# Kernel optimization log

Hardware: AMD Instinct MI355X
Metric: run time of the kernel (lower is better)

## Reference

```python
import jax, jax.numpy as jnp
import numpy as np

T, B, I, H, L = 1024, 64, 512, 512, 2


def _gru_layer(x_seq, h0, w_ih, w_hh, b_ih, b_hh):
    # x_seq: [T, B, in], h0: [B, H]
    # Precompute input-side gates for all timesteps in one big GEMM.
    gx = jnp.einsum('tbi,gi->tbg', x_seq, w_ih) + b_ih  # [T, B, 3H]

    def step(h, gx_t):
        gh = h @ w_hh.T + b_hh                 # [B, 3H]
        i_r, i_z, i_n = jnp.split(gx_t, 3, axis=-1)
        h_r, h_z, h_n = jnp.split(gh, 3, axis=-1)
        r = jax.nn.sigmoid(i_r + h_r)
        z = jax.nn.sigmoid(i_z + h_z)
        n = jnp.tanh(i_n + r * h_n)
        hy = n + z * (h - n)                   # newgate + inputgate*(hx - newgate)
        return hy, hy

    hT, out = jax.lax.scan(step, h0, gx)
    return out, hT  # out: [T, B, H]


def setup_inputs() -> dict:
    key = jax.random.key(0)
    ks = jax.random.split(key, 10)
    stdv = 1.0 / np.sqrt(H)
    u = lambda k, shp: jax.random.uniform(k, shp, jnp.float32, -stdv, stdv)
    return {
        'x': jax.random.normal(ks[0], (T, B, I), jnp.float32),
        'hx': jax.random.normal(ks[1], (L, B, H), jnp.float32),
        'w_ih_0': u(ks[2], (3 * H, I)),
        'w_hh_0': u(ks[3], (3 * H, H)),
        'b_ih_0': u(ks[4], (3 * H,)),
        'b_hh_0': u(ks[5], (3 * H,)),
        'w_ih_1': u(ks[6], (3 * H, H)),
        'w_hh_1': u(ks[7], (3 * H, H)),
        'b_ih_1': u(ks[8], (3 * H,)),
        'b_hh_1': u(ks[9], (3 * H,)),
    }


def reference(x, hx, w_ih_0, w_hh_0, b_ih_0, b_hh_0, w_ih_1, w_hh_1, b_ih_1, b_hh_1):
    out0, h0T = _gru_layer(x, hx[0], w_ih_0, w_hh_0, b_ih_0, b_hh_0)
    out1, h1T = _gru_layer(out0, hx[1], w_ih_1, w_hh_1, b_ih_1, b_hh_1)
    output = out1                         # [T, B, H] (batch_first=False)
    output_hs = jnp.stack([h0T, h1T], 0)  # [L, B, H]
    return output, output_hs
```

## Files before the change

### kernel.cpp

```cpp
#include <hip/hip_runtime.h>
#include <cstdint>
#include <cstddef>

#define T_N 1024
#define B_N 64
#define I_N 512
#define H_N 512
#define G3  (3*H_N)
#define NBLK 256

typedef _Float16 f16;
typedef _Float16 f16x2 __attribute__((ext_vector_type(2)));
typedef unsigned long long ull;

#define SLOT(d) (((d)+2)&1)
#define TAG1(d) ((((d)+2)>>1)&1)

__device__ __forceinline__ f16x2 mkh2(float a, float b) {
  f16x2 v; v.x = (_Float16)a; v.y = (_Float16)b; return v;
}
__device__ __forceinline__ f16x2 bch2(unsigned int u) {
  return __builtin_bit_cast(f16x2, u);
}
__device__ __forceinline__ float fdot2_(f16x2 a, f16x2 b, float c) {
#if __has_builtin(__builtin_amdgcn_fdot2)
  return __builtin_amdgcn_fdot2(a, b, c, false);
#else
  return fmaf((float)a.x, (float)b.x, fmaf((float)a.y, (float)b.y, c));
#endif
}
__device__ __forceinline__ float sigm_(float x) { return 1.f / (1.f + __expf(-x)); }
__device__ __forceinline__ float tanhf_(float x) {
  float xx = fminf(15.f, fmaxf(-15.f, x));
  float e = __expf(2.f * xx);
  return (e - 1.f) / (e + 1.f);
}

__global__ __launch_bounds__(256) void gemm_nt(
    const float* __restrict__ A,
    const float* __restrict__ W,
    const float* __restrict__ bias,
    float* __restrict__ C,
    int M, int N, int K)
{
  __shared__ float As[32][68];
  __shared__ float Ws[32][68];
  const int tid = threadIdx.x;
  const int n0 = blockIdx.x * 64;
  const int m0 = blockIdx.y * 64;
  const int ty = tid >> 4;
  const int tx = tid & 15;

  float acc[4][4];
#pragma unroll
  for (int i = 0; i < 4; ++i)
#pragma unroll
    for (int jj = 0; jj < 4; ++jj) acc[i][jj] = 0.f;

  for (int k0 = 0; k0 < K; k0 += 32) {
#pragma unroll
    for (int i = 0; i < 2; ++i) {
      int idx = tid + i * 256;
      int r   = idx >> 3;
      int c4  = idx & 7;
      float4 va = *(const float4*)(A + (size_t)(m0 + r) * K + k0 + c4 * 4);
      As[c4*4+0][r] = va.x; As[c4*4+1][r] = va.y;
      As[c4*4+2][r] = va.z; As[c4*4+3][r] = va.w;
      float4 vw = *(const float4*)(W + (size_t)(n0 + r) * K + k0 + c4 * 4);
      Ws[c4*4+0][r] = vw.x; Ws[c4*4+1][r] = vw.y;
      Ws[c4*4+2][r] = vw.z; Ws[c4*4+3][r] = vw.w;
    }
    __syncthreads();
#pragma unroll
    for (int k = 0; k < 32; ++k) {
      float4 a = *(const float4*)&As[k][ty * 4];
      float4 w = *(const float4*)&Ws[k][tx * 4];
      acc[0][0] += a.x*w.x; acc[0][1] += a.x*w.y; acc[0][2] += a.x*w.z; acc[0][3] += a.x*w.w;
      acc[1][0] += a.y*w.x; acc[1][1] += a.y*w.y; acc[1][2] += a.y*w.z; acc[1][3] += a.y*w.w;
      acc[2][0] += a.z*w.x; acc[2][1] += a.z*w.y; acc[2][2] += a.z*w.z; acc[2][3] += a.z*w.w;
      acc[3][0] += a.w*w.x; acc[3][1] += a.w*w.y; acc[3][2] += a.w*w.z; acc[3][3] += a.w*w.w;
    }
    __syncthreads();
  }

  float4 bv = *(const float4*)(bias + n0 + tx * 4);
#pragma unroll
  for (int i = 0; i < 4; ++i) {
    int row = m0 + ty * 4 + i;
    float4 o;
    o.x = acc[i][0] + bv.x; o.y = acc[i][1] + bv.y;
    o.z = acc[i][2] + bv.z; o.w = acc[i][3] + bv.w;
    *(float4*)(C + (size_t)row * N + n0 + tx * 4) = o;
  }
}

__global__ __launch_bounds__(256) void pack_h_init(
    const float* __restrict__ hx, f16* __restrict__ h0x, f16* __restrict__ h1x)
{
  int i = blockIdx.x * 256 + threadIdx.x;
  unsigned short a = __builtin_bit_cast(unsigned short, (f16)hx[i]) & 0xFFFEu;
  unsigned short b = __builtin_bit_cast(unsigned short, (f16)hx[B_N * H_N + i]) & 0xFFFEu;
  ((unsigned short*)h0x)[B_N * H_N + i] = a;
  ((unsigned short*)h1x)[B_N * H_N + i] = b;
}

__global__ __launch_bounds__(256) void conv_w(
    const float* __restrict__ whh0, const float* __restrict__ wih1,
    const float* __restrict__ whh1, uint4* __restrict__ wbuf)
{
  int gid = blockIdx.x * 256 + threadIdx.x;
  int idx = gid % 18, rem = gid / 18;
  int tid = rem % 512, j = rem / 512;
  int u = tid >> 5, s = tid & 31;
  int mat = idx / 6, q = (idx % 6) / 2, c = idx % 2;
  const float* src = mat == 0 ? whh0 : (mat == 1 ? wih1 : whh1);
  const float* p = src + (size_t)(q * H_N + 16 * j + u) * H_N + 16 * s + 8 * c;
  uint4 o;
  o.x = __builtin_bit_cast(unsigned int, mkh2(p[0], p[1]));
  o.y = __builtin_bit_cast(unsigned int, mkh2(p[2], p[3]));
  o.z = __builtin_bit_cast(unsigned int, mkh2(p[4], p[5]));
  o.w = __builtin_bit_cast(unsigned int, mkh2(p[6], p[7]));
  wbuf[gid] = o;
}

#define D4Q(acc, wv, vv)                               \
  acc = fdot2_(bch2((wv).x), bch2((vv).x), acc);       \
  acc = fdot2_(bch2((wv).y), bch2((vv).y), acc);       \
  acc = fdot2_(bch2((wv).z), bch2((vv).z), acc);       \
  acc = fdot2_(bch2((wv).w), bch2((vv).w), acc);

template <int NQ>
__device__ __forceinline__ void rscat8w(float a[][8], float* r, int s) {
#pragma unroll
  for (int q = 0; q < NQ; ++q) {
    float k4[4];
#pragma unroll
    for (int i = 0; i < 4; ++i) {
      float snd = (s & 1) ? a[q][i] : a[q][4 + i];
      float kp  = (s & 1) ? a[q][4 + i] : a[q][i];
      k4[i] = kp + __shfl_xor(snd, 1);
    }
    float k2[2];
#pragma unroll
    for (int i = 0; i < 2; ++i) {
      float snd = (s & 2) ? k4[i] : k4[2 + i];
      float kp  = (s & 2) ? k4[2 + i] : k4[i];
      k2[i] = kp + __shfl_xor(snd, 2);
    }
    float snd = (s & 4) ? k2[0] : k2[1];
    float kp  = (s & 4) ? k2[1] : k2[0];
    float k1 = kp + __shfl_xor(snd, 4);
    k1 = k1 + __shfl_xor(k1, 8);
    r[q] = k1 + __shfl_xor(k1, 16);
  }
}

__global__ __launch_bounds__(512, 2) void gru_fused(
    const float* __restrict__ gx,
    const float* __restrict__ hx,
    const uint4* __restrict__ wbuf,
    const float* __restrict__ bih1, const float* __restrict__ bhh0,
    const float* __restrict__ bhh1,
    float* __restrict__ out,
    float* __restrict__ hT,
    f16* __restrict__ h0x, f16* __restrict__ h1x)
{
  __shared__ __align__(16) ull sh0q[2][1024];
  __shared__ __align__(16) ull sh1q[1024];
  __shared__ __align__(8) unsigned short pkA[128], pkB[128];

  const int tid = threadIdx.x;
  const int bid = blockIdx.x;
  const int g = bid & 7;
  const int j = bid >> 3;
  const int u = tid >> 5;
  const int s = tid & 31;
  const ull M = 0x0001000100010001ULL;

  uint4 wq[18];
  {
    const uint4* wp = wbuf + ((size_t)j * 512 + tid) * 18;
#pragma unroll
    for (int i = 0; i < 18; ++i) wq[i] = wp[i];
#pragma unroll
    for (int i = 0; i < 18; ++i)
      asm volatile("" : "+v"(wq[i].x), "+v"(wq[i].y), "+v"(wq[i].z), "+v"(wq[i].w));
  }

  const int bb   = 4 * (s & 1) + 2 * ((s >> 1) & 1) + ((s >> 2) & 1);
  const int unit = 16 * j + u;
  const int gbi  = 8 * g + bb;
  const bool wr  = (s < 8);
  float bR0 = 0, bZ0 = 0, bN0 = 0, bR1 = 0, bZ1 = 0, bN1x = 0, bN1h = 0;
  float hv0 = 0, hv1 = 0;
  if (wr) {
    bR0 = bhh0[unit]; bZ0 = bhh0[H_N + unit]; bN0 = bhh0[2 * H_N + unit];
    bR1 = bih1[unit] + bhh1[unit];
    bZ1 = bih1[H_N + unit] + bhh1[H_N + unit];
    bN1x = bih1[2 * H_N + unit]; bN1h = bhh1[2 * H_N + unit];
    hv0 = hx[(size_t)gbi * H_N + unit];
    hv1 = hx[(size_t)(B_N + gbi) * H_N + unit];
  }

  for (int t = 0; t <= T_N + 1; ++t) {
    const bool runA = (t < T_N);
    const bool pollH0 = (t <= T_N);
    const bool runB = (t >= 2);
    const int cur = t & 1;

    const ull* s0 = (const ull*)h0x + (size_t)SLOT(t - 1) * 8192 + (size_t)(8 * g) * 128;
    const ull* s1 = (const ull*)h1x + (size_t)SLOT(t - 3) * 8192 + (size_t)(8 * g) * 128;
    const ull e0 = TAG1(t - 1) ? M : 0ULL;
    const ull e1 = TAG1(t - 3) ? M : 0ULL;
    ull v0[2], v1[2];
    bool k0[2] = {false, false};
    if (pollH0) {
#pragma unroll
      for (int e = 0; e < 2; ++e)
        v0[e] = __hip_atomic_load(s0 + e * 512 + tid, __ATOMIC_RELAXED, __HIP_MEMORY_SCOPE_AGENT);
    }
    if (runB) {
#pragma unroll
      for (int e = 0; e < 2; ++e)
        v1[e] = __hip_atomic_load(s1 + e * 512 + tid, __ATOMIC_RELAXED, __HIP_MEMORY_SCOPE_AGENT);
    }

    float ir0 = 0, iz0 = 0, in0 = 0;
    if (runA && wr) {
      const float* p = gx + ((size_t)t * B_N + gbi) * G3 + unit;
      ir0 = p[0]; iz0 = p[H_N]; in0 = p[2 * H_N];
    }

    if (runB) {
      bool k1[2] = {false, false};
      for (;;) {
        bool all = true;
#pragma unroll
        for (int e = 0; e < 2; ++e) {
          if (!k1[e]) k1[e] = ((v1[e] & M) == e1);
          all = all && k1[e];
        }
        if (__all(all)) break;
        __builtin_amdgcn_s_sleep(1);
#pragma unroll
        for (int e = 0; e < 2; ++e)
          if (!k1[e]) v1[e] = __hip_atomic_load(s1 + e * 512 + tid, __ATOMIC_RELAXED, __HIP_MEMORY_SCOPE_AGENT);
      }
#pragma unroll
      for (int e = 0; e < 2; ++e) sh1q[e * 512 + tid] = v1[e];
    }
    __syncthreads();

    if (runB) {
      float aB[4][8];
#pragma unroll
      for (int q = 0; q < 4; ++q)
#pragma unroll
        for (int b8 = 0; b8 < 8; ++b8) aB[q][b8] = 0.f;
      const uint4* xp = (const uint4*)sh0q[cur ^ 1];
      const uint4* hp = (const uint4*)sh1q;
#pragma unroll
      for (int b8 = 0; b8 < 8; ++b8) {
        uint4 xc[2], hc[2];
#pragma unroll
        for (int c = 0; c < 2; ++c) {
          xc[c] = xp[b8 * 64 + 2 * s + c];
          hc[c] = hp[b8 * 64 + 2 * s + c];
        }
        float a0 = aB[0][b8], a1 = aB[1][b8], a2 = aB[2][b8], a3 = aB[3][b8];
#pragma unroll
        for (int c = 0; c < 2; ++c) {
          D4Q(a0, wq[6 + c],  xc[c]); D4Q(a0, wq[12 + c], hc[c]);
          D4Q(a1, wq[8 + c],  xc[c]); D4Q(a1, wq[14 + c], hc[c]);
          D4Q(a2, wq[10 + c], xc[c]);
          D4Q(a3, wq[16 + c], hc[c]);
        }
        aB[0][b8] = a0; aB[1][b8] = a1; aB[2][b8] = a2; aB[3][b8] = a3;
      }
      float rB[4];
      rscat8w<4>(aB, rB, s);
      if (wr) {
        float r = sigm_(rB[0] + bR1);
        float z = sigm_(rB[1] + bZ1);
        float n = tanhf_(rB[2] + bN1x + r * (rB[3] + bN1h));
        float hy = n + z * (hv1 - n); hv1 = hy;
        pkB[bb * 16 + u] = __builtin_bit_cast(unsigned short, (f16)hy);
      }
    }

    if (pollH0) {
      for (;;) {
        bool all = true;
#pragma unroll
        for (int e = 0; e < 2; ++e) {
          if (!k0[e]) k0[e] = ((v0[e] & M) == e0);
          all = all && k0[e];
        }
        if (__all(all)) break;
        __builtin_amdgcn_s_sleep(1);
#pragma unroll
        for (int e = 0; e < 2; ++e)
          if (!k0[e]) v0[e] = __hip_atomic_load(s0 + e * 512 + tid, __ATOMIC_RELAXED, __HIP_MEMORY_SCOPE_AGENT);
      }
#pragma unroll
      for (int e = 0; e < 2; ++e) sh0q[cur][e * 512 + tid] = v0[e];
    }
    __syncthreads();

    if (runA) {
      float aA[3][8];
#pragma unroll
      for (int q = 0; q < 3; ++q)
#pragma unroll
        for (int b8 = 0; b8 < 8; ++b8) aA[q][b8] = 0.f;
      const uint4* xp = (const uint4*)sh0q[cur];
#pragma unroll
      for (int b8 = 0; b8 < 8; ++b8) {
        uint4 xc[2];
        xc[0] = xp[b8 * 64 + 2 * s];
        xc[1] = xp[b8 * 64 + 2 * s + 1];
        float a0 = aA[0][b8], a1 = aA[1][b8], a2 = aA[2][b8];
#pragma unroll
        for (int c = 0; c < 2; ++c) {
          D4Q(a0, wq[0 + c], xc[c]);
          D4Q(a1, wq[2 + c], xc[c]);
          D4Q(a2, wq[4 + c], xc[c]);
        }
        aA[0][b8] = a0; aA[1][b8] = a1; aA[2][b8] = a2;
      }
      float rA[3];
      rscat8w<3>(aA, rA, s);
      if (wr) {
        float r = sigm_(ir0 + rA[0] + bR0);
        float z = sigm_(iz0 + rA[1] + bZ0);
        float n = tanhf_(in0 + r * (rA[2] + bN0));
        float hy = n + z * (hv0 - n); hv0 = hy;
        pkA[bb * 16 + u] = __builtin_bit_cast(unsigned short, (f16)hy);
        if (t == T_N - 1) hT[(size_t)gbi * H_N + unit] = hy;
      }
    }
    __syncthreads();

    if (tid < 32) {
      if (runA) {
        ull v = ((const ull*)pkA)[tid];
        v = (v & ~M) | (TAG1(t) ? M : 0ULL);
        ull* dp = (ull*)h0x + (size_t)SLOT(t) * 8192
                + (size_t)(8 * g + (tid >> 2)) * 128 + 4 * j + (tid & 3);
        __hip_atomic_store(dp, v, __ATOMIC_RELAXED, __HIP_MEMORY_SCOPE_AGENT);
      }
    } else if (tid < 64) {
      if (runB) {
        const int l = tid - 32;
        ull v = ((const ull*)pkB)[l];
        f16x2 p0 = bch2((unsigned int)v), p1 = bch2((unsigned int)(v >> 32));
        float4 o = {(float)p0.x, (float)p0.y, (float)p1.x, (float)p1.y};
        float* op = out + ((size_t)(t - 2) * B_N + 8 * g + (l >> 2)) * H_N + 16 * j + 4 * (l & 3);
        *(float4*)op = o;
        if (t == T_N + 1)
          *(float4*)(hT + (size_t)(B_N + 8 * g + (l >> 2)) * H_N + 16 * j + 4 * (l & 3)) = o;
        if (t <= T_N) {
          v = (v & ~M) | (TAG1(t - 2) ? M : 0ULL);
          ull* dp = (ull*)h1x + (size_t)SLOT(t - 2) * 8192
                  + (size_t)(8 * g + (l >> 2)) * 128 + 4 * j + (l & 3);
          __hip_atomic_store(dp, v, __ATOMIC_RELAXED, __HIP_MEMORY_SCOPE_AGENT);
        }
      }
    }
  }
}

extern "C" void kernel_launch(void* const* d_in, const int* in_sizes, int n_in,
                              void* d_out, int out_size, void* d_ws, size_t ws_size,
                              hipStream_t stream)
{
  const float* x    = (const float*)d_in[0];
  const float* hx   = (const float*)d_in[1];
  const float* wih0 = (const float*)d_in[2];
  const float* whh0 = (const float*)d_in[3];
  const float* bih0 = (const float*)d_in[4];
  const float* bhh0 = (const float*)d_in[5];
  const float* wih1 = (const float*)d_in[6];
  const float* whh1 = (const float*)d_in[7];
  const float* bih1 = (const float*)d_in[8];
  const float* bhh1 = (const float*)d_in[9];
  float* out = (float*)d_out;

  float* gxb = (float*)d_ws;
  f16*   h0x = (f16*)(gxb + (size_t)T_N * B_N * G3);
  f16*   h1x = h0x + 2 * B_N * H_N;
  uint4* wbuf = (uint4*)(h1x + 2 * B_N * H_N);

  pack_h_init<<<128, 256, 0, stream>>>(hx, h0x, h1x);
  conv_w<<<(32 * 512 * 18) / 256, 256, 0, stream>>>(whh0, wih1, whh1, wbuf);

  dim3 gg(G3 / 64, (T_N * B_N) / 64);
  gemm_nt<<<gg, 256, 0, stream>>>(x, wih0, bih0, gxb, T_N * B_N, G3, I_N);

  gru_fused<<<NBLK, 512, 0, stream>>>(gxb, hx, wbuf,
                                      bih1, bhh0, bhh1,
                                      out, out + (size_t)T_N * B_N * H_N,
                                      h0x, h1x);
}
```

Before: 10.01 ms.

## Move layer-1 weights from registers to LDS and reinterleave K slicing

Keeps only the six layer-0 recurrent weight vectors in registers and stages the twelve layer-1 weight vectors in shared memory, read once per c-chunk inside the layer-1 dot product. The weight packing and activation reads change from each lane owning 16 contiguous elements to two 8-element chunks strided by 256, which is meant to spread LDS accesses across banks. The min-blocks-per-CU hint is dropped from launch bounds, relaxing the register cap. This lowers VGPR pressure and spills at the cost of extra LDS traffic and a less unrolled layer-1 loop on the serial recurrence path.

```diff
diff --git a/kernel.cpp b/kernel.cpp
--- a/kernel.cpp
+++ b/kernel.cpp
@@ -114,7 +114,7 @@
   int u = tid >> 5, s = tid & 31;
   int mat = idx / 6, q = (idx % 6) / 2, c = idx % 2;
   const float* src = mat == 0 ? whh0 : (mat == 1 ? wih1 : whh1);
-  const float* p = src + (size_t)(q * H_N + 16 * j + u) * H_N + 16 * s + 8 * c;
+  const float* p = src + (size_t)(q * H_N + 16 * j + u) * H_N + 8 * s + 256 * c;
   uint4 o;
   o.x = __builtin_bit_cast(unsigned int, mkh2(p[0], p[1]));
   o.y = __builtin_bit_cast(unsigned int, mkh2(p[2], p[3]));
@@ -155,7 +155,23 @@
   }
 }
 
-__global__ __launch_bounds__(512, 2) void gru_fused(
+#define POLL2(vv, kk, sp, ee)                                                  \
+  for (;;) {                                                                   \
+    bool all_ = true;                                                          \
+    _Pragma("unroll")                                                          \
+    for (int e_ = 0; e_ < 2; ++e_) {                                           \
+      if (!kk[e_]) kk[e_] = ((vv[e_] & M) == ee);                              \
+      all_ = all_ && kk[e_];                                                   \
+    }                                                                          \
+    if (__all(all_)) break;                                                    \
+    __builtin_amdgcn_s_sleep(1);                                               \
+    _Pragma("unroll")                                                          \
+    for (int e_ = 0; e_ < 2; ++e_)                                             \
+      if (!kk[e_]) vv[e_] = __hip_atomic_load(sp + e_ * 512 + tid,             \
+                     __ATOMIC_RELAXED, __HIP_MEMORY_SCOPE_AGENT);              \
+  }
+
+__global__ __launch_bounds__(512) void gru_fused(
     const float* __restrict__ gx,
     const float* __restrict__ hx,
     const uint4* __restrict__ wbuf,
@@ -165,6 +181,7 @@
     float* __restrict__ hT,
     f16* __restrict__ h0x, f16* __restrict__ h1x)
 {
+  __shared__ __align__(16) uint4 wl[12 * 512];
   __shared__ __align__(16) ull sh0q[2][1024];
   __shared__ __align__(16) ull sh1q[1024];
   __shared__ __align__(8) unsigned short pkA[128], pkB[128];
@@ -177,22 +194,24 @@
   const int s = tid & 31;
   const ull M = 0x0001000100010001ULL;
 
-  uint4 wq[18];
+  uint4 wq[6];
   {
     const uint4* wp = wbuf + ((size_t)j * 512 + tid) * 18;
 #pragma unroll
-    for (int i = 0; i < 18; ++i) wq[i] = wp[i];
-#pragma unroll
-    for (int i = 0; i < 18; ++i)
-      asm volatile("" : "+v"(wq[i].x), "+v"(wq[i].y), "+v"(wq[i].z), "+v"(wq[i].w));
+    for (int i = 0; i < 6; ++i) wq[i] = wp[i];
+#pragma unroll
+    for (int i = 0; i < 12; ++i) wl[i * 512 + tid] = wp[6 + i];
   }
 
   const int bb   = 4 * (s & 1) + 2 * ((s >> 1) & 1) + ((s >> 2) & 1);
   const int unit = 16 * j + u;
   const int gbi  = 8 * g + bb;
   const bool wr  = (s < 8);
-  float bR0 = 0, bZ0 = 0, bN0 = 0, bR1 = 0, bZ1 = 0, bN1x = 0, bN1h = 0;
-  float hv0 = 0, hv1 = 0;
+  const ull* h0u = (const ull*)h0x;
+  const ull* h1u = (const ull*)h1x;
+
+  float bR0 = 0, bZ0 = 0, bN0 = 0, hv0 = 0;
+  float bR1 = 0, bZ1 = 0, bN1x = 0, bN1h = 0, hv1 = 0;
   if (wr) {
     bR0 = bhh0[unit]; bZ0 = bhh0[H_N + unit]; bN0 = bhh0[2 * H_N + unit];
     bR1 = bih1[unit] + bhh1[unit];
@@ -201,6 +220,7 @@
     hv0 = hx[(size_t)gbi * H_N + unit];
     hv1 = hx[(size_t)(B_N + gbi) * H_N + unit];
   }
+  __syncthreads();
 
   for (int t = 0; t <= T_N + 1; ++t) {
     const bool runA = (t < T_N);
@@ -208,8 +228,8 @@
     const bool runB = (t >= 2);
     const int cur = t & 1;
 
-    const ull* s0 = (const ull*)h0x + (size_t)SLOT(t - 1) * 8192 + (size_t)(8 * g) * 128;
-    const ull* s1 = (const ull*)h1x + (size_t)SLOT(t - 3) * 8192 + (size_t)(8 * g) * 128;
+    const ull* s0 = h0u + (size_t)SLOT(t - 1) * 8192 + (size_t)(8 * g) * 128;
+    const ull* s1 = h1u + (size_t)SLOT(t - 3) * 8192 + (size_t)(8 * g) * 128;
     const ull e0 = TAG1(t - 1) ? M : 0ULL;
     const ull e1 = TAG1(t - 3) ? M : 0ULL;
     ull v0[2], v1[2];
@@ -233,19 +253,7 @@
 
     if (runB) {
       bool k1[2] = {false, false};
-      for (;;) {
-        bool all = true;
-#pragma unroll
-        for (int e = 0; e < 2; ++e) {
-          if (!k1[e]) k1[e] = ((v1[e] & M) == e1);
-          all = all && k1[e];
-        }
-        if (__all(all)) break;
-        __builtin_amdgcn_s_sleep(1);
-#pragma unroll
-        for (int e = 0; e < 2; ++e)
-          if (!k1[e]) v1[e] = __hip_atomic_load(s1 + e * 512 + tid, __ATOMIC_RELAXED, __HIP_MEMORY_SCOPE_AGENT);
-      }
+      POLL2(v1, k1, s1, e1)
 #pragma unroll
       for (int e = 0; e < 2; ++e) sh1q[e * 512 + tid] = v1[e];
     }
@@ -259,23 +267,23 @@
         for (int b8 = 0; b8 < 8; ++b8) aB[q][b8] = 0.f;
       const uint4* xp = (const uint4*)sh0q[cur ^ 1];
       const uint4* hp = (const uint4*)sh1q;
-#pragma unroll
-      for (int b8 = 0; b8 < 8; ++b8) {
-        uint4 xc[2], hc[2];
-#pragma unroll
-        for (int c = 0; c < 2; ++c) {
-          xc[c] = xp[b8 * 64 + 2 * s + c];
-          hc[c] = hp[b8 * 64 + 2 * s + c];
+#pragma unroll 1
+      for (int c = 0; c < 2; ++c) {
+        uint4 wx0 = wl[(0 * 2 + c) * 512 + tid];
+        uint4 wx1 = wl[(1 * 2 + c) * 512 + tid];
+        uint4 wx2 = wl[(2 * 2 + c) * 512 + tid];
+        uint4 wh0 = wl[(6 + 0 * 2 + c) * 512 + tid];
+        uint4 wh1 = wl[(6 + 1 * 2 + c) * 512 + tid];
+        uint4 wh2 = wl[(6 + 2 * 2 + c) * 512 + tid];
+#pragma unroll
+        for (int b8 = 0; b8 < 8; ++b8) {
+          uint4 x = xp[b8 * 64 + s + 32 * c];
+          uint4 h = hp[b8 * 64 + s + 32 * c];
+          D4Q(aB[0][b8], wx0, x); D4Q(aB[0][b8], wh0, h);
+          D4Q(aB[1][b8], wx1, x); D4Q(aB[1][b8], wh1, h);
+          D4Q(aB[2][b8], wx2, x);
+          D4Q(aB[3][b8], wh2, h);
         }
-        float a0 = aB[0][b8], a1 = aB[1][b8], a2 = aB[2][b8], a3 = aB[3][b8];
-#pragma unroll
-        for (int c = 0; c < 2; ++c) {
-          D4Q(a0, wq[6 + c],  xc[c]); D4Q(a0, wq[12 + c], hc[c]);
-          D4Q(a1, wq[8 + c],  xc[c]); D4Q(a1, wq[14 + c], hc[c]);
-          D4Q(a2, wq[10 + c], xc[c]);
-          D4Q(a3, wq[16 + c], hc[c]);
-        }
-        aB[0][b8] = a0; aB[1][b8] = a1; aB[2][b8] = a2; aB[3][b8] = a3;
       }
       float rB[4];
       rscat8w<4>(aB, rB, s);
@@ -289,19 +297,7 @@
     }
 
     if (pollH0) {
-      for (;;) {
-        bool all = true;
-#pragma unroll
-        for (int e = 0; e < 2; ++e) {
-          if (!k0[e]) k0[e] = ((v0[e] & M) == e0);
-          all = all && k0[e];
-        }
-        if (__all(all)) break;
-        __builtin_amdgcn_s_sleep(1);
-#pragma unroll
-        for (int e = 0; e < 2; ++e)
-          if (!k0[e]) v0[e] = __hip_atomic_load(s0 + e * 512 + tid, __ATOMIC_RELAXED, __HIP_MEMORY_SCOPE_AGENT);
-      }
+      POLL2(v0, k0, s0, e0)
 #pragma unroll
       for (int e = 0; e < 2; ++e) sh0q[cur][e * 512 + tid] = v0[e];
     }
@@ -317,8 +313,8 @@
 #pragma unroll
       for (int b8 = 0; b8 < 8; ++b8) {
         uint4 xc[2];
-        xc[0] = xp[b8 * 64 + 2 * s];
-        xc[1] = xp[b8 * 64 + 2 * s + 1];
+        xc[0] = xp[b8 * 64 + s];
+        xc[1] = xp[b8 * 64 + s + 32];
         float a0 = aA[0][b8], a1 = aA[1][b8], a2 = aA[2][b8];
 #pragma unroll
         for (int c = 0; c < 2; ++c) {
```

Result: faster. 9.622 ms (-3.8%).
